# Optimization experiments

Measured on AMD Instinct MI355X. Metric: run time of the kernel, lower is better.

## Reference

```python
import jax, jax.numpy as jnp
import numpy as np

B = 4            # scenes
N = 100000       # points per scene
BN = B * N
M = 200000       # occupied target voxels
C_IMG = 64       # img_feat_dim
C_3D = 32        # INIT_DIM (3D feature width at p1 scale)
COORD_MAX = 256  # voxel grid extent per axis


def setup_inputs() -> dict:
    key = jax.random.key(0)
    k1, k2, k3, k4, k5, k6 = jax.random.split(key, 6)
    # batched voxel coords: col0 = batch idx, cols1:4 = xyz voxel coords
    bcol = jax.random.randint(k1, (M, 1), 0, B, dtype=jnp.int32)
    xyz = jax.random.randint(k2, (M, 3), 0, COORD_MAX, dtype=jnp.int32)
    tgt_coords = jnp.concatenate([bcol, xyz], axis=1)  # (M,4)
    # each point maps onto some target voxel (torch code asserts full validity)
    pts_idx = jax.random.randint(k3, (BN,), 0, M, dtype=jnp.int32)
    pfeat = jax.random.normal(k4, (BN, C_IMG), dtype=jnp.float32)
    tgt_feats = jax.random.normal(k5, (M, C_3D), dtype=jnp.float32)
    W_fuse = jax.random.normal(k6, (C_3D + C_IMG, C_3D), dtype=jnp.float32) * 0.05
    b_fuse = jnp.zeros((C_3D,), dtype=jnp.float32)
    return {"pfeat": pfeat, "tgt_feats": tgt_feats, "W_fuse": W_fuse,
            "b_fuse": b_fuse, "tgt_coords": tgt_coords, "pts_idx": pts_idx}


def reference(pfeat, tgt_feats, W_fuse, b_fuse, tgt_coords, pts_idx):
    # point voxel coords (stride-snapped in torch; identity here since points map to voxels)
    pts_coords = tgt_coords[pts_idx]                              # (BN,4)
    # --- key packing (mirrors _pack_keys with shift-to-nonnegative) ---
    xyz_all = jnp.concatenate([pts_coords[:, 1:], tgt_coords[:, 1:]], axis=0)
    shift = jnp.maximum(-xyz_all.min(axis=0), 0)
    pts_xyz = pts_coords[:, 1:] + shift
    tgt_xyz = tgt_coords[:, 1:] + shift
    max_xyz = jnp.maximum(pts_xyz.max(axis=0), tgt_xyz.max(axis=0))
    mx, my, mz = max_xyz[0] + 1, max_xyz[1] + 1, max_xyz[2] + 1

    def pack(b, xyz):
        return ((b * mx + xyz[:, 0]) * my + xyz[:, 1]) * mz + xyz[:, 2]

    pts_key = pack(pts_coords[:, 0], pts_xyz)                     # (BN,)
    tgt_key = pack(tgt_coords[:, 0], tgt_xyz)                     # (M,)
    # --- sort target keys, binary-search point keys (torch.sort + searchsorted) ---
    order = jnp.argsort(tgt_key)
    tgt_key_sorted = tgt_key[order]
    pos = jnp.minimum(jnp.searchsorted(tgt_key_sorted, pts_key), M - 1)
    tgt_idx = order[pos]                                          # (BN,) voxel each point lands in
    # --- scatter-mean of 2D point features into voxels (_scatter_mean) ---
    sums = jax.ops.segment_sum(pfeat, tgt_idx, num_segments=M)    # (M,C_IMG)
    cnt = jax.ops.segment_sum(jnp.ones((pfeat.shape[0], 1), pfeat.dtype),
                              tgt_idx, num_segments=M)            # (M,1)
    img_feat_u = sums / jnp.maximum(cnt, 1.0)
    # --- ME.cat + 1x1 MinkowskiConvolution fuse == concat + matmul ---
    fused = jnp.concatenate([tgt_feats, img_feat_u], axis=1)      # (M, C_3D+C_IMG)
    return fused @ W_fuse + b_fuse                                # (M, C_3D)
```

## Files before the change

### kernel.cpp

```cpp
#include <hip/hip_runtime.h>

#define HBITS 19
#define HSIZE (1u << HBITS)
#define HMASK (HSIZE - 1u)
#define EMPTY_KEY 0xFFFFFFFFu
#define SLOTS 8

__device__ __forceinline__ unsigned hash_key(unsigned k) {
    return (k * 2654435761u) >> (32 - HBITS);
}

__device__ __forceinline__ unsigned pack_key(int4 c) {
    return ((unsigned)c.x << 24) | ((unsigned)c.y << 16) |
           ((unsigned)c.z << 8) | (unsigned)c.w;
}

__global__ __launch_bounds__(256)
void build_hash(const int4* __restrict__ tgt_coords, int M,
                uint2* __restrict__ htab) {
    int v = blockIdx.x * blockDim.x + threadIdx.x;
    if (v >= M) return;
    unsigned key = pack_key(tgt_coords[v]);
    unsigned h = hash_key(key);
    while (true) {
        unsigned prev = atomicCAS(&htab[h].x, EMPTY_KEY, key);
        if (prev == EMPTY_KEY || prev == key) {
            atomicMin(&htab[h].y, (unsigned)v);
            break;
        }
        h = (h + 1u) & HMASK;
    }
}

__global__ __launch_bounds__(256)
void fill_slots(const int* __restrict__ pts_idx,
                const int4* __restrict__ tgt_coords,
                const uint2* __restrict__ htab,
                int BN,
                int* __restrict__ cnt,
                int* __restrict__ slotbuf,
                int* __restrict__ ohead,
                int* __restrict__ nxt) {
    int p = blockIdx.x * blockDim.x + threadIdx.x;
    if (p >= BN) return;
    int vox = pts_idx[p];
    unsigned key = pack_key(tgt_coords[vox]);
    unsigned h = hash_key(key);
    uint2 e = htab[h];
    while (e.x != key) { h = (h + 1u) & HMASK; e = htab[h]; }
    int c = (int)e.y;
    int idx = atomicAdd(&cnt[c], 1) + 1;
    if (idx < SLOTS) slotbuf[c * SLOTS + idx] = p;
    else             nxt[p] = atomicExch(&ohead[c], p);
}

#define VPB 8
__global__ __launch_bounds__(256)
void fuse_bucket(const float2* __restrict__ pf2,
                 const int* __restrict__ cnt,
                 const int4* __restrict__ slot4,
                 const int* __restrict__ ohead,
                 const int* __restrict__ nxt,
                 const float* __restrict__ tgt_feats,
                 const float* __restrict__ W,
                 const float* __restrict__ bias,
                 int M,
                 float* __restrict__ out) {
    __shared__ float Ws[96 * 32];
    __shared__ float bs[32];
    __shared__ __align__(16) float xbuf[VPB][96];

    int t = threadIdx.x;
    for (int i = t; i < 96 * 32; i += 256) Ws[i] = W[i];
    if (t < 32) bs[t] = bias[t];

    int grp = t >> 5;
    int g   = t & 31;
    int v = blockIdx.x * VPB + grp;
    bool valid = v < M;

    float sx = 0.0f, sy = 0.0f;
    int n = 0;
    if (valid) {
        n = cnt[v] + 1;
        int4 sa = make_int4(0, 0, 0, 0), sb = make_int4(0, 0, 0, 0);
        if (n > 0) sa = slot4[(size_t)v * 2];
        if (n > 4) sb = slot4[(size_t)v * 2 + 1];
        float2 f0 = {0,0}, f1 = {0,0}, f2 = {0,0}, f3 = {0,0};
        float2 f4 = {0,0}, f5 = {0,0}, f6 = {0,0}, f7 = {0,0};
        if (n > 0) f0 = pf2[(size_t)sa.x * 32 + g];
        if (n > 1) f1 = pf2[(size_t)sa.y * 32 + g];
        if (n > 2) f2 = pf2[(size_t)sa.z * 32 + g];
        if (n > 3) f3 = pf2[(size_t)sa.w * 32 + g];
        if (n > 4) f4 = pf2[(size_t)sb.x * 32 + g];
        if (n > 5) f5 = pf2[(size_t)sb.y * 32 + g];
        if (n > 6) f6 = pf2[(size_t)sb.z * 32 + g];
        if (n > 7) f7 = pf2[(size_t)sb.w * 32 + g];
        sx = ((f0.x + f1.x) + (f2.x + f3.x)) + ((f4.x + f5.x) + (f6.x + f7.x));
        sy = ((f0.y + f1.y) + (f2.y + f3.y)) + ((f4.y + f5.y) + (f6.y + f7.y));
        if (n > SLOTS) {
            int p = ohead[v];
            while (p >= 0) {
                float2 f = pf2[(size_t)p * 32 + g];
                sx += f.x; sy += f.y;
                p = nxt[p];
            }
        }
    }
    float inv = 1.0f / fmaxf((float)n, 1.0f);

    if (valid) {
        xbuf[grp][32 + 2 * g]     = sx * inv;
        xbuf[grp][32 + 2 * g + 1] = sy * inv;
        if (g < 16) {
            float2 tf = ((const float2*)tgt_feats)[(size_t)v * 16 + g];
            xbuf[grp][2 * g]     = tf.x;
            xbuf[grp][2 * g + 1] = tf.y;
        }
    }
    __syncthreads();
    if (!valid) return;

    float acc = bs[g];
#pragma unroll
    for (int k4 = 0; k4 < 24; ++k4) {
        float4 x = *(const float4*)&xbuf[grp][k4 * 4];
        acc = fmaf(x.x, Ws[(k4 * 4 + 0) * 32 + g], acc);
        acc = fmaf(x.y, Ws[(k4 * 4 + 1) * 32 + g], acc);
        acc = fmaf(x.z, Ws[(k4 * 4 + 2) * 32 + g], acc);
        acc = fmaf(x.w, Ws[(k4 * 4 + 3) * 32 + g], acc);
    }
    out[(size_t)v * 32 + g] = acc;
}

extern "C" void kernel_launch(void* const* d_in, const int* in_sizes, int n_in,
                              void* d_out, int out_size, void* d_ws, size_t ws_size,
                              hipStream_t stream) {
    const float* pfeat      = (const float*)d_in[0];
    const float* tgt_feats  = (const float*)d_in[1];
    const float* W_fuse     = (const float*)d_in[2];
    const float* b_fuse     = (const float*)d_in[3];
    const int*   tgt_coords = (const int*)d_in[4];
    const int*   pts_idx    = (const int*)d_in[5];
    float* out = (float*)d_out;

    const int M  = in_sizes[4] / 4;
    const int BN = in_sizes[5];

    char* ws = (char*)d_ws;
    uint2* htab    = (uint2*)ws;
    int*   cnt     = (int*)(ws + (size_t)HSIZE * 8);
    int*   ohead   = (int*)(ws + (size_t)HSIZE * 8 + (size_t)M * 4);
    int*   slotbuf = (int*)(ws + (size_t)HSIZE * 8 + (size_t)M * 8);
    int*   nxt     = (int*)(ws + (size_t)HSIZE * 8 + (size_t)M * 8 + (size_t)M * SLOTS * 4);

    size_t ff_bytes = (size_t)HSIZE * 8 + (size_t)M * 8;
    hipMemsetAsync(htab, 0xFF, ff_bytes, stream);

    const int TB = 256;
    build_hash<<<(M + TB - 1) / TB, TB, 0, stream>>>(
        (const int4*)tgt_coords, M, htab);
    fill_slots<<<(BN + TB - 1) / TB, TB, 0, stream>>>(
        pts_idx, (const int4*)tgt_coords, htab, BN, cnt, slotbuf, ohead, nxt);
    fuse_bucket<<<(M + VPB - 1) / VPB, TB, 0, stream>>>(
        (const float2*)pfeat, cnt, (const int4*)slotbuf, ohead, nxt,
        tgt_feats, W_fuse, b_fuse, M, out);
}
```

Before: 313.1 us.

## Process 8 voxels per warp with register-tiled fuse matmul

The fuse kernel now gives each 32-lane group eight voxels instead of one, so a block covers 64 voxels. Gathered means and target features are staged into a padded shared buffer. The 96x32 weight is stored transposed with padding, so each lane loads its weights once per k-step and reuses them across the eight accumulators. This cuts the per-block weight staging cost and the shared-memory weight reads per output. In exchange, the gather loop per lane becomes serial over eight voxels, there are eight times fewer blocks, and register and LDS use rise.

Result: slower. 965.0 us (+208.2%).

```diff
diff --git a/kernel.cpp b/kernel.cpp
--- a/kernel.cpp
+++ b/kernel.cpp
@@ -54,35 +54,39 @@
     else             nxt[p] = atomicExch(&ohead[c], p);
 }
 
-#define VPB 8
+#define VGRP 8
+#define XPAD 100
+#define WPAD 98
 __global__ __launch_bounds__(256)
-void fuse_bucket(const float2* __restrict__ pf2,
-                 const int* __restrict__ cnt,
-                 const int4* __restrict__ slot4,
-                 const int* __restrict__ ohead,
-                 const int* __restrict__ nxt,
-                 const float* __restrict__ tgt_feats,
-                 const float* __restrict__ W,
-                 const float* __restrict__ bias,
-                 int M,
-                 float* __restrict__ out) {
-    __shared__ float Ws[96 * 32];
-    __shared__ float bs[32];
-    __shared__ __align__(16) float xbuf[VPB][96];
+void fuse_reg(const float2* __restrict__ pf2,
+              const int* __restrict__ cnt,
+              const int4* __restrict__ slot4,
+              const int* __restrict__ ohead,
+              const int* __restrict__ nxt,
+              const float* __restrict__ tgt_feats,
+              const float* __restrict__ W,
+              const float* __restrict__ bias,
+              int M,
+              float* __restrict__ out) {
+    __shared__ __align__(16) float xbuf[64 * XPAD];
+    __shared__ __align__(16) float Wt[32 * WPAD];
 
     int t = threadIdx.x;
-    for (int i = t; i < 96 * 32; i += 256) Ws[i] = W[i];
-    if (t < 32) bs[t] = bias[t];
+    for (int i = t; i < 96 * 32; i += 256) {
+        int k = i >> 5, oc = i & 31;
+        Wt[oc * WPAD + k] = W[i];
+    }
 
     int grp = t >> 5;
     int g   = t & 31;
-    int v = blockIdx.x * VPB + grp;
-    bool valid = v < M;
+    int vbase = blockIdx.x * 64 + grp * VGRP;
+    float bval = bias[g];
 
-    float sx = 0.0f, sy = 0.0f;
-    int n = 0;
-    if (valid) {
-        n = cnt[v] + 1;
+#pragma unroll
+    for (int vv = 0; vv < VGRP; ++vv) {
+        int v = vbase + vv;
+        if (v >= M) break;
+        int n = cnt[v] + 1;
         int4 sa = make_int4(0, 0, 0, 0), sb = make_int4(0, 0, 0, 0);
         if (n > 0) sa = slot4[(size_t)v * 2];
         if (n > 4) sb = slot4[(size_t)v * 2 + 1];
@@ -96,8 +100,8 @@
         if (n > 5) f5 = pf2[(size_t)sb.y * 32 + g];
         if (n > 6) f6 = pf2[(size_t)sb.z * 32 + g];
         if (n > 7) f7 = pf2[(size_t)sb.w * 32 + g];
-        sx = ((f0.x + f1.x) + (f2.x + f3.x)) + ((f4.x + f5.x) + (f6.x + f7.x));
-        sy = ((f0.y + f1.y) + (f2.y + f3.y)) + ((f4.y + f5.y) + (f6.y + f7.y));
+        float sx = ((f0.x + f1.x) + (f2.x + f3.x)) + ((f4.x + f5.x) + (f6.x + f7.x));
+        float sy = ((f0.y + f1.y) + (f2.y + f3.y)) + ((f4.y + f5.y) + (f6.y + f7.y));
         if (n > SLOTS) {
             int p = ohead[v];
             while (p >= 0) {
@@ -106,31 +110,38 @@
                 p = nxt[p];
             }
         }
-    }
-    float inv = 1.0f / fmaxf((float)n, 1.0f);
-
-    if (valid) {
-        xbuf[grp][32 + 2 * g]     = sx * inv;
-        xbuf[grp][32 + 2 * g + 1] = sy * inv;
+        float inv = 1.0f / fmaxf((float)n, 1.0f);
+        int row = (grp * VGRP + vv) * XPAD;
+        *(float2*)&xbuf[row + 32 + 2 * g] = make_float2(sx * inv, sy * inv);
         if (g < 16) {
             float2 tf = ((const float2*)tgt_feats)[(size_t)v * 16 + g];
-            xbuf[grp][2 * g]     = tf.x;
-            xbuf[grp][2 * g + 1] = tf.y;
+            *(float2*)&xbuf[row + 2 * g] = tf;
         }
     }
     __syncthreads();
-    if (!valid) return;
 
-    float acc = bs[g];
+    float acc[VGRP];
+#pragma unroll
+    for (int vv = 0; vv < VGRP; ++vv) acc[vv] = bval;
+
 #pragma unroll
     for (int k4 = 0; k4 < 24; ++k4) {
-        float4 x = *(const float4*)&xbuf[grp][k4 * 4];
-        acc = fmaf(x.x, Ws[(k4 * 4 + 0) * 32 + g], acc);
-        acc = fmaf(x.y, Ws[(k4 * 4 + 1) * 32 + g], acc);
-        acc = fmaf(x.z, Ws[(k4 * 4 + 2) * 32 + g], acc);
-        acc = fmaf(x.w, Ws[(k4 * 4 + 3) * 32 + g], acc);
+        float2 w01 = *(const float2*)&Wt[g * WPAD + k4 * 4];
+        float2 w23 = *(const float2*)&Wt[g * WPAD + k4 * 4 + 2];
+#pragma unroll
+        for (int vv = 0; vv < VGRP; ++vv) {
+            float4 x = *(const float4*)&xbuf[(grp * VGRP + vv) * XPAD + k4 * 4];
+            acc[vv] = fmaf(x.x, w01.x, acc[vv]);
+            acc[vv] = fmaf(x.y, w01.y, acc[vv]);
+            acc[vv] = fmaf(x.z, w23.x, acc[vv]);
+            acc[vv] = fmaf(x.w, w23.y, acc[vv]);
+        }
     }
-    out[(size_t)v * 32 + g] = acc;
+#pragma unroll
+    for (int vv = 0; vv < VGRP; ++vv) {
+        int v = vbase + vv;
+        if (v < M) out[(size_t)v * 32 + g] = acc[vv];
+    }
 }
 
 extern "C" void kernel_launch(void* const* d_in, const int* in_sizes, int n_in,
@@ -162,7 +173,7 @@
         (const int4*)tgt_coords, M, htab);
     fill_slots<<<(BN + TB - 1) / TB, TB, 0, stream>>>(
         pts_idx, (const int4*)tgt_coords, htab, BN, cnt, slotbuf, ohead, nxt);
-    fuse_bucket<<<(M + VPB - 1) / VPB, TB, 0, stream>>>(
+    fuse_reg<<<(M + 63) / 64, TB, 0, stream>>>(
         (const float2*)pfeat, cnt, (const int4*)slotbuf, ohead, nxt,
         tgt_feats, W_fuse, b_fuse, M, out);
 }
```

## Use persistent wave-per-voxel fuse kernel with register-resident weights

Applied to the files above, without the earlier changes.

Replaces the one-voxel-per-32-thread-group fuse kernel with a persistent grid of 1024 blocks. Each 64-lane wave grid-strides over voxels and keeps its half of the 96x32 weight matrix in 48 registers. The K dimension is split across the two half-waves and combined with a cross-lane shuffle. This removes the per-block shared-memory weight reload and the block barrier, and it gathers point features with one float per lane. The cost is higher register pressure. There is also an intra-wave write-then-read of xbuf through LDS with no barrier, which relies on wave-synchronous execution.

After: 319.9 us. 1.02x slower.

```diff
diff --git a/kernel.cpp b/kernel.cpp
--- a/kernel.cpp
+++ b/kernel.cpp
@@ -54,83 +54,77 @@
     else             nxt[p] = atomicExch(&ohead[c], p);
 }
 
-#define VPB 8
 __global__ __launch_bounds__(256)
-void fuse_bucket(const float2* __restrict__ pf2,
-                 const int* __restrict__ cnt,
-                 const int4* __restrict__ slot4,
-                 const int* __restrict__ ohead,
-                 const int* __restrict__ nxt,
-                 const float* __restrict__ tgt_feats,
-                 const float* __restrict__ W,
-                 const float* __restrict__ bias,
-                 int M,
-                 float* __restrict__ out) {
-    __shared__ float Ws[96 * 32];
-    __shared__ float bs[32];
-    __shared__ __align__(16) float xbuf[VPB][96];
+void fuse_wave(const float* __restrict__ pf,
+               const int* __restrict__ cnt,
+               const int4* __restrict__ slot4,
+               const int* __restrict__ ohead,
+               const int* __restrict__ nxt,
+               const float* __restrict__ tgt_feats,
+               const float* __restrict__ W,
+               const float* __restrict__ bias,
+               int M,
+               float* __restrict__ out) {
+    __shared__ __align__(16) float xbuf[4][96];
 
     int t = threadIdx.x;
-    for (int i = t; i < 96 * 32; i += 256) Ws[i] = W[i];
-    if (t < 32) bs[t] = bias[t];
+    int wid = t >> 6;
+    int l   = t & 63;
+    int oc  = l & 31;
+    int kh  = l >> 5;
 
-    int grp = t >> 5;
-    int g   = t & 31;
-    int v = blockIdx.x * VPB + grp;
-    bool valid = v < M;
+    float wreg[48];
+#pragma unroll
+    for (int j = 0; j < 48; ++j) wreg[j] = W[(kh * 48 + j) * 32 + oc];
+    float bval = bias[oc];
 
-    float sx = 0.0f, sy = 0.0f;
-    int n = 0;
-    if (valid) {
-        n = cnt[v] + 1;
+    float* xrow = &xbuf[wid][0];
+    const float4* xr4 = (const float4*)(xrow + kh * 48);
+
+    int gwave  = blockIdx.x * 4 + wid;
+    int nwaves = gridDim.x * 4;
+
+#pragma unroll 1
+    for (int v = gwave; v < M; v += nwaves) {
+        int n = cnt[v] + 1;
         int4 sa = make_int4(0, 0, 0, 0), sb = make_int4(0, 0, 0, 0);
         if (n > 0) sa = slot4[(size_t)v * 2];
         if (n > 4) sb = slot4[(size_t)v * 2 + 1];
-        float2 f0 = {0,0}, f1 = {0,0}, f2 = {0,0}, f3 = {0,0};
-        float2 f4 = {0,0}, f5 = {0,0}, f6 = {0,0}, f7 = {0,0};
-        if (n > 0) f0 = pf2[(size_t)sa.x * 32 + g];
-        if (n > 1) f1 = pf2[(size_t)sa.y * 32 + g];
-        if (n > 2) f2 = pf2[(size_t)sa.z * 32 + g];
-        if (n > 3) f3 = pf2[(size_t)sa.w * 32 + g];
-        if (n > 4) f4 = pf2[(size_t)sb.x * 32 + g];
-        if (n > 5) f5 = pf2[(size_t)sb.y * 32 + g];
-        if (n > 6) f6 = pf2[(size_t)sb.z * 32 + g];
-        if (n > 7) f7 = pf2[(size_t)sb.w * 32 + g];
-        sx = ((f0.x + f1.x) + (f2.x + f3.x)) + ((f4.x + f5.x) + (f6.x + f7.x));
-        sy = ((f0.y + f1.y) + (f2.y + f3.y)) + ((f4.y + f5.y) + (f6.y + f7.y));
+        float f0 = 0.f, f1 = 0.f, f2 = 0.f, f3 = 0.f;
+        float f4 = 0.f, f5 = 0.f, f6 = 0.f, f7 = 0.f;
+        if (n > 0) f0 = pf[(size_t)sa.x * 64 + l];
+        if (n > 1) f1 = pf[(size_t)sa.y * 64 + l];
+        if (n > 2) f2 = pf[(size_t)sa.z * 64 + l];
+        if (n > 3) f3 = pf[(size_t)sa.w * 64 + l];
+        if (n > 4) f4 = pf[(size_t)sb.x * 64 + l];
+        if (n > 5) f5 = pf[(size_t)sb.y * 64 + l];
+        if (n > 6) f6 = pf[(size_t)sb.z * 64 + l];
+        if (n > 7) f7 = pf[(size_t)sb.w * 64 + l];
+        float s = ((f0 + f1) + (f2 + f3)) + ((f4 + f5) + (f6 + f7));
         if (n > SLOTS) {
             int p = ohead[v];
             while (p >= 0) {
-                float2 f = pf2[(size_t)p * 32 + g];
-                sx += f.x; sy += f.y;
+                s += pf[(size_t)p * 64 + l];
                 p = nxt[p];
             }
         }
+        float inv = 1.0f / fmaxf((float)n, 1.0f);
+
+        xrow[32 + l] = s * inv;
+        if (l < 32) xrow[l] = tgt_feats[(size_t)v * 32 + l];
+
+        float acc = 0.0f;
+#pragma unroll
+        for (int k4 = 0; k4 < 12; ++k4) {
+            float4 x = xr4[k4];
+            acc = fmaf(x.x, wreg[k4 * 4 + 0], acc);
+            acc = fmaf(x.y, wreg[k4 * 4 + 1], acc);
+            acc = fmaf(x.z, wreg[k4 * 4 + 2], acc);
+            acc = fmaf(x.w, wreg[k4 * 4 + 3], acc);
+        }
+        acc += __shfl_xor(acc, 32, 64);
+        if (l < 32) out[(size_t)v * 32 + oc] = acc + bval;
     }
-    float inv = 1.0f / fmaxf((float)n, 1.0f);
-
-    if (valid) {
-        xbuf[grp][32 + 2 * g]     = sx * inv;
-        xbuf[grp][32 + 2 * g + 1] = sy * inv;
-        if (g < 16) {
-            float2 tf = ((const float2*)tgt_feats)[(size_t)v * 16 + g];
-            xbuf[grp][2 * g]     = tf.x;
-            xbuf[grp][2 * g + 1] = tf.y;
-        }
-    }
-    __syncthreads();
-    if (!valid) return;
-
-    float acc = bs[g];
-#pragma unroll
-    for (int k4 = 0; k4 < 24; ++k4) {
-        float4 x = *(const float4*)&xbuf[grp][k4 * 4];
-        acc = fmaf(x.x, Ws[(k4 * 4 + 0) * 32 + g], acc);
-        acc = fmaf(x.y, Ws[(k4 * 4 + 1) * 32 + g], acc);
-        acc = fmaf(x.z, Ws[(k4 * 4 + 2) * 32 + g], acc);
-        acc = fmaf(x.w, Ws[(k4 * 4 + 3) * 32 + g], acc);
-    }
-    out[(size_t)v * 32 + g] = acc;
 }
 
 extern "C" void kernel_launch(void* const* d_in, const int* in_sizes, int n_in,
@@ -162,7 +156,7 @@
         (const int4*)tgt_coords, M, htab);
     fill_slots<<<(BN + TB - 1) / TB, TB, 0, stream>>>(
         pts_idx, (const int4*)tgt_coords, htab, BN, cnt, slotbuf, ohead, nxt);
-    fuse_bucket<<<(M + VPB - 1) / VPB, TB, 0, stream>>>(
-        (const float2*)pfeat, cnt, (const int4*)slotbuf, ohead, nxt,
+    fuse_wave<<<1024, TB, 0, stream>>>(
+        pfeat, cnt, (const int4*)slotbuf, ohead, nxt,
         tgt_feats, W_fuse, b_fuse, M, out);
 }
```

## Split fused gather+matmul into gather-mean kernel and per-row scalar matmul kernel

Applied to the files above, without the earlier changes.

Unfuses the scatter-mean gather from the 1x1 fuse matmul. Gathered means are written to a workspace buffer, and a separate kernel gives each thread one voxel row and keeps 32 accumulators in registers. Weights are read through uniform global loads instead of being staged in LDS per block. This removes the per-block weight load into LDS and the block barrier, at the cost of an extra round trip of M*64 floats through global memory and one more kernel launch.

Measured after the change: 287.5 us. 1.09x faster.

```diff
diff --git a/kernel.cpp b/kernel.cpp
--- a/kernel.cpp
+++ b/kernel.cpp
@@ -56,81 +56,92 @@
 
 #define VPB 8
 __global__ __launch_bounds__(256)
-void fuse_bucket(const float2* __restrict__ pf2,
+void gather_mean(const float2* __restrict__ pf2,
                  const int* __restrict__ cnt,
                  const int4* __restrict__ slot4,
                  const int* __restrict__ ohead,
                  const int* __restrict__ nxt,
-                 const float* __restrict__ tgt_feats,
-                 const float* __restrict__ W,
-                 const float* __restrict__ bias,
                  int M,
-                 float* __restrict__ out) {
-    __shared__ float Ws[96 * 32];
-    __shared__ float bs[32];
-    __shared__ __align__(16) float xbuf[VPB][96];
-
+                 float2* __restrict__ mean2) {
     int t = threadIdx.x;
-    for (int i = t; i < 96 * 32; i += 256) Ws[i] = W[i];
-    if (t < 32) bs[t] = bias[t];
-
     int grp = t >> 5;
     int g   = t & 31;
     int v = blockIdx.x * VPB + grp;
-    bool valid = v < M;
+    if (v >= M) return;
 
-    float sx = 0.0f, sy = 0.0f;
-    int n = 0;
-    if (valid) {
-        n = cnt[v] + 1;
-        int4 sa = make_int4(0, 0, 0, 0), sb = make_int4(0, 0, 0, 0);
-        if (n > 0) sa = slot4[(size_t)v * 2];
-        if (n > 4) sb = slot4[(size_t)v * 2 + 1];
-        float2 f0 = {0,0}, f1 = {0,0}, f2 = {0,0}, f3 = {0,0};
-        float2 f4 = {0,0}, f5 = {0,0}, f6 = {0,0}, f7 = {0,0};
-        if (n > 0) f0 = pf2[(size_t)sa.x * 32 + g];
-        if (n > 1) f1 = pf2[(size_t)sa.y * 32 + g];
-        if (n > 2) f2 = pf2[(size_t)sa.z * 32 + g];
-        if (n > 3) f3 = pf2[(size_t)sa.w * 32 + g];
-        if (n > 4) f4 = pf2[(size_t)sb.x * 32 + g];
-        if (n > 5) f5 = pf2[(size_t)sb.y * 32 + g];
-        if (n > 6) f6 = pf2[(size_t)sb.z * 32 + g];
-        if (n > 7) f7 = pf2[(size_t)sb.w * 32 + g];
-        sx = ((f0.x + f1.x) + (f2.x + f3.x)) + ((f4.x + f5.x) + (f6.x + f7.x));
-        sy = ((f0.y + f1.y) + (f2.y + f3.y)) + ((f4.y + f5.y) + (f6.y + f7.y));
-        if (n > SLOTS) {
-            int p = ohead[v];
-            while (p >= 0) {
-                float2 f = pf2[(size_t)p * 32 + g];
-                sx += f.x; sy += f.y;
-                p = nxt[p];
-            }
+    int n = cnt[v] + 1;
+    int4 sa = make_int4(0, 0, 0, 0), sb = make_int4(0, 0, 0, 0);
+    if (n > 0) sa = slot4[(size_t)v * 2];
+    if (n > 4) sb = slot4[(size_t)v * 2 + 1];
+    float2 f0 = {0,0}, f1 = {0,0}, f2 = {0,0}, f3 = {0,0};
+    float2 f4 = {0,0}, f5 = {0,0}, f6 = {0,0}, f7 = {0,0};
+    if (n > 0) f0 = pf2[(size_t)sa.x * 32 + g];
+    if (n > 1) f1 = pf2[(size_t)sa.y * 32 + g];
+    if (n > 2) f2 = pf2[(size_t)sa.z * 32 + g];
+    if (n > 3) f3 = pf2[(size_t)sa.w * 32 + g];
+    if (n > 4) f4 = pf2[(size_t)sb.x * 32 + g];
+    if (n > 5) f5 = pf2[(size_t)sb.y * 32 + g];
+    if (n > 6) f6 = pf2[(size_t)sb.z * 32 + g];
+    if (n > 7) f7 = pf2[(size_t)sb.w * 32 + g];
+    float sx = ((f0.x + f1.x) + (f2.x + f3.x)) + ((f4.x + f5.x) + (f6.x + f7.x));
+    float sy = ((f0.y + f1.y) + (f2.y + f3.y)) + ((f4.y + f5.y) + (f6.y + f7.y));
+    if (n > SLOTS) {
+        int p = ohead[v];
+        while (p >= 0) {
+            float2 f = pf2[(size_t)p * 32 + g];
+            sx += f.x; sy += f.y;
+            p = nxt[p];
         }
     }
     float inv = 1.0f / fmaxf((float)n, 1.0f);
+    mean2[(size_t)v * 32 + g] = make_float2(sx * inv, sy * inv);
+}
 
-    if (valid) {
-        xbuf[grp][32 + 2 * g]     = sx * inv;
-        xbuf[grp][32 + 2 * g + 1] = sy * inv;
-        if (g < 16) {
-            float2 tf = ((const float2*)tgt_feats)[(size_t)v * 16 + g];
-            xbuf[grp][2 * g]     = tf.x;
-            xbuf[grp][2 * g + 1] = tf.y;
+__global__ __launch_bounds__(256)
+void matmul_scalar(const float4* __restrict__ tgt4,
+                   const float4* __restrict__ mean4,
+                   const float* __restrict__ W,
+                   const float* __restrict__ bias,
+                   int M,
+                   float4* __restrict__ out4) {
+    int v = blockIdx.x * blockDim.x + threadIdx.x;
+    if (v >= M) return;
+
+    float acc[32];
+#pragma unroll
+    for (int oc = 0; oc < 32; ++oc) acc[oc] = bias[oc];
+
+    const float4* xr = tgt4 + (size_t)v * 8;
+#pragma unroll 2
+    for (int k4 = 0; k4 < 8; ++k4) {
+        float4 x = xr[k4];
+        const float* w0 = W + k4 * 4 * 32;
+#pragma unroll
+        for (int oc = 0; oc < 32; ++oc) {
+            acc[oc] = fmaf(x.x, w0[oc],      acc[oc]);
+            acc[oc] = fmaf(x.y, w0[32 + oc], acc[oc]);
+            acc[oc] = fmaf(x.z, w0[64 + oc], acc[oc]);
+            acc[oc] = fmaf(x.w, w0[96 + oc], acc[oc]);
         }
     }
-    __syncthreads();
-    if (!valid) return;
+    const float4* mr = mean4 + (size_t)v * 16;
+#pragma unroll 2
+    for (int k4 = 0; k4 < 16; ++k4) {
+        float4 x = mr[k4];
+        const float* w0 = W + (32 + k4 * 4) * 32;
+#pragma unroll
+        for (int oc = 0; oc < 32; ++oc) {
+            acc[oc] = fmaf(x.x, w0[oc],      acc[oc]);
+            acc[oc] = fmaf(x.y, w0[32 + oc], acc[oc]);
+            acc[oc] = fmaf(x.z, w0[64 + oc], acc[oc]);
+            acc[oc] = fmaf(x.w, w0[96 + oc], acc[oc]);
+        }
+    }
 
-    float acc = bs[g];
+    float4* o = out4 + (size_t)v * 8;
 #pragma unroll
-    for (int k4 = 0; k4 < 24; ++k4) {
-        float4 x = *(const float4*)&xbuf[grp][k4 * 4];
-        acc = fmaf(x.x, Ws[(k4 * 4 + 0) * 32 + g], acc);
-        acc = fmaf(x.y, Ws[(k4 * 4 + 1) * 32 + g], acc);
-        acc = fmaf(x.z, Ws[(k4 * 4 + 2) * 32 + g], acc);
-        acc = fmaf(x.w, Ws[(k4 * 4 + 3) * 32 + g], acc);
-    }
-    out[(size_t)v * 32 + g] = acc;
+    for (int q = 0; q < 8; ++q)
+        o[q] = make_float4(acc[4 * q], acc[4 * q + 1], acc[4 * q + 2], acc[4 * q + 3]);
 }
 
 extern "C" void kernel_launch(void* const* d_in, const int* in_sizes, int n_in,
@@ -149,10 +160,12 @@
 
     char* ws = (char*)d_ws;
     uint2* htab    = (uint2*)ws;
-    int*   cnt     = (int*)(ws + (size_t)HSIZE * 8);
-    int*   ohead   = (int*)(ws + (size_t)HSIZE * 8 + (size_t)M * 4);
-    int*   slotbuf = (int*)(ws + (size_t)HSIZE * 8 + (size_t)M * 8);
-    int*   nxt     = (int*)(ws + (size_t)HSIZE * 8 + (size_t)M * 8 + (size_t)M * SLOTS * 4);
+    size_t off = (size_t)HSIZE * 8;
+    int*   cnt     = (int*)(ws + off);              off += (size_t)M * 4;
+    int*   ohead   = (int*)(ws + off);              off += (size_t)M * 4;
+    int*   slotbuf = (int*)(ws + off);              off += (size_t)M * SLOTS * 4;
+    int*   nxt     = (int*)(ws + off);              off += (size_t)BN * 4;
+    float* mean    = (float*)(ws + off);
 
     size_t ff_bytes = (size_t)HSIZE * 8 + (size_t)M * 8;
     hipMemsetAsync(htab, 0xFF, ff_bytes, stream);
@@ -162,7 +175,10 @@
         (const int4*)tgt_coords, M, htab);
     fill_slots<<<(BN + TB - 1) / TB, TB, 0, stream>>>(
         pts_idx, (const int4*)tgt_coords, htab, BN, cnt, slotbuf, ohead, nxt);
-    fuse_bucket<<<(M + VPB - 1) / VPB, TB, 0, stream>>>(
-        (const float2*)pfeat, cnt, (const int4*)slotbuf, ohead, nxt,
-        tgt_feats, W_fuse, b_fuse, M, out);
+    gather_mean<<<(M + VPB - 1) / VPB, TB, 0, stream>>>(
+        (const float2*)pfeat, cnt, (const int4*)slotbuf, ohead, nxt, M,
+        (float2*)mean);
+    matmul_scalar<<<(M + TB - 1) / TB, TB, 0, stream>>>(
+        (const float4*)tgt_feats, (const float4*)mean, W_fuse, b_fuse, M,
+        (float4*)out);
 }
```
